# Kernel optimization log

Measured on AMD Instinct MI355X. Metric: run time of the kernel, lower is better.

Reference implementation:

```python
import jax, jax.numpy as jnp
import numpy as np

D_MODEL = 1024
N_HEAD = 16
L, B = 2048, 2


def setup_inputs() -> dict:
    key = jax.random.key(0)
    ks = jax.random.split(key, 11)
    inp = {
        "q": jax.random.normal(ks[0], (L, B, D_MODEL), dtype=jnp.float32),
        "k": jax.random.normal(ks[1], (L, B, D_MODEL), dtype=jnp.float32),
        "v": jax.random.normal(ks[2], (L, B, D_MODEL), dtype=jnp.float32),
        "sph": jax.random.uniform(ks[3], (B, N_HEAD, L, L), dtype=jnp.float32),
        "mask": jax.random.randint(ks[4], (B, L, L), 0, 2, dtype=jnp.int32),
        # learned params (torch Linear stores W of shape [out, in]; y = x @ W.T)
        "Wq": jax.random.normal(ks[5], (D_MODEL, D_MODEL), dtype=jnp.float32) * (1.0 / np.sqrt(D_MODEL)),
        "Wk": jax.random.normal(ks[6], (D_MODEL, D_MODEL), dtype=jnp.float32) * (1.0 / np.sqrt(D_MODEL)),
        "Wv": jax.random.normal(ks[7], (D_MODEL, D_MODEL), dtype=jnp.float32) * (1.0 / np.sqrt(D_MODEL)),
        "Wfc": jax.random.normal(ks[8], (D_MODEL, D_MODEL), dtype=jnp.float32) * (1.0 / np.sqrt(D_MODEL)),
        "gamma": jnp.ones((D_MODEL,), dtype=jnp.float32),
        "beta": jnp.zeros((D_MODEL,), dtype=jnp.float32),
    }
    return inp


def reference(q, k, v, sph, mask, Wq, Wk, Wv, Wfc, gamma, beta):
    # q, k, v: [L, B, D]  ->  batch-first [B, L, D]
    n_head = N_HEAD
    Lq, Bb, D = q.shape
    d_k = D // n_head
    x_q = jnp.transpose(q, (1, 0, 2))
    x_k = jnp.transpose(k, (1, 0, 2))
    x_v = jnp.transpose(v, (1, 0, 2))
    residual = x_q  # [B, L, D]

    # projections (no bias), split heads: [B, H, L, d_k]
    qh = (x_q @ Wq.T).reshape(Bb, Lq, n_head, d_k).transpose(0, 2, 1, 3)
    kh = (x_k @ Wk.T).reshape(Bb, Lq, n_head, d_k).transpose(0, 2, 1, 3)
    vh = (x_v @ Wv.T).reshape(Bb, Lq, n_head, d_k).transpose(0, 2, 1, 3)

    scale = jnp.asarray(d_k, qh.dtype) ** 0.5
    attn = jnp.einsum('bhqd,bhkd->bhqk', qh / scale, kh)
    attn = attn * sph                                   # spatial decay modulation
    attn = jnp.where(mask[:, None, :, :] == 0, jnp.asarray(-1e9, attn.dtype), attn)
    p_attn = jax.nn.softmax(attn, axis=-1)              # dropout is identity in eval

    out = jnp.einsum('bhqk,bhkd->bhqd', p_attn, vh)     # [B, H, L, d_k]
    out = out.transpose(0, 2, 1, 3).reshape(Bb, Lq, D)
    out = out @ Wfc.T + residual                        # fc (no bias) + residual

    # LayerNorm(eps=1e-6)
    mu = jnp.mean(out, axis=-1, keepdims=True)
    var = jnp.var(out, axis=-1, keepdims=True)
    out = (out - mu) * jax.lax.rsqrt(var + 1e-6) * gamma + beta

    return jnp.transpose(out, (1, 0, 2)), p_attn
```

## Files before the change

kernel.cpp:

```cpp
#include <hip/hip_runtime.h>
#include <hip/hip_bf16.h>

#define LL 2048
#define BB 2
#define DD 1024
#define HH 16
#define DKk 64

typedef __attribute__((ext_vector_type(8))) short s8v;
typedef __attribute__((ext_vector_type(8))) unsigned short u8v;
typedef __attribute__((ext_vector_type(4))) float f4v;

__device__ __forceinline__ ushort f2b(float f){
  union { __hip_bfloat16 h; ushort u; } c; c.h = __float2bfloat16(f); return c.u;
}
__device__ __forceinline__ float b2f(ushort u){
  union { __hip_bfloat16 h; ushort u; } c; c.u = u; return __bfloat162float(c.h);
}
__device__ __forceinline__ void nts4(float* p, f4v v){ __builtin_nontemporal_store(v, (f4v*)p); }

__global__ __launch_bounds__(256) void pack_all_kernel(
    const float* __restrict__ q, const float* __restrict__ k, const float* __restrict__ v,
    const float* __restrict__ Wq, const float* __restrict__ Wk,
    const float* __restrict__ Wv, const float* __restrict__ Wfc,
    const int* __restrict__ mask,
    ushort* __restrict__ xq, ushort* __restrict__ xk, ushort* __restrict__ xv,
    ushort* __restrict__ wb, unsigned* __restrict__ mbitsT){
  int blk = blockIdx.x;
  if (blk < 2048){
    int t = blk*256 + threadIdx.x;
    int m = t >> 7;
    int dc = (t & 127) << 3;
    int b = m >> 11, l = m & (LL-1);
    size_t src = ((size_t)(l*BB + b) << 10) + dc;
    size_t dst = ((size_t)m << 10) + dc;
    #pragma unroll
    for (int i=0;i<3;++i){
      const float* ss = (i==0)?q:(i==1)?k:v;
      ushort* dd = (i==0)?xq:(i==1)?xk:xv;
      float4 a = *(const float4*)(ss+src);
      float4 bb = *(const float4*)(ss+src+4);
      u8v o;
      o[0]=f2b(a.x); o[1]=f2b(a.y); o[2]=f2b(a.z); o[3]=f2b(a.w);
      o[4]=f2b(bb.x);o[5]=f2b(bb.y);o[6]=f2b(bb.z);o[7]=f2b(bb.w);
      *(u8v*)(dd+dst) = o;
    }
  } else if (blk < 4096){
    int t = (blk-2048)*256 + threadIdx.x;
    int which = t >> 17;
    size_t idx = (size_t)(t & 131071) << 3;
    const float* s = (which==0)?Wq:(which==1)?Wk:(which==2)?Wv:Wfc;
    float4 a = *(const float4*)(s+idx);
    float4 b4 = *(const float4*)(s+idx+4);
    u8v o;
    o[0]=f2b(a.x);o[1]=f2b(a.y);o[2]=f2b(a.z);o[3]=f2b(a.w);
    o[4]=f2b(b4.x);o[5]=f2b(b4.y);o[6]=f2b(b4.z);o[7]=f2b(b4.w);
    *(u8v*)(wb + ((size_t)which<<20) + idx) = o;
  } else {
    int t = (blk-4096)*256 + threadIdx.x;
    int rowg = t >> 6, lane = t & 63;
    const int* mrow = mask + ((size_t)rowg<<11);
    unsigned mw = 0;
    #pragma unroll
    for (int c=0;c<4;++c){
      const int* p = mrow + (c<<9) + (lane<<3);
      int4 a = *(const int4*)p; int4 b4 = *(const int4*)(p+4);
      unsigned by = (a.x&1)|((a.y&1)<<1)|((a.z&1)<<2)|((a.w&1)<<3)
                  |((b4.x&1)<<4)|((b4.y&1)<<5)|((b4.z&1)<<6)|((b4.w&1)<<7);
      mw |= by << (c*8);
    }
    mbitsT[((size_t)rowg<<6) + lane] = mw;
  }
}

__device__ __forceinline__ void gemm_body(
    const ushort* __restrict__ A, const ushort* __restrict__ W,
    ushort* __restrict__ outb, float* __restrict__ outf, const float* __restrict__ resid,
    int mode, float scale){
  __shared__ ushort As[4096];
  __shared__ ushort Bs[4096];
  int tid = threadIdx.x;
  int w = tid>>6, lane = tid&63, lane15 = lane&15, g = lane>>4;
  int m0 = blockIdx.y<<7, n0 = blockIdx.x<<7;
  int wr = w>>1, wc = w&1;
  f4v z4 = {0.f,0.f,0.f,0.f};
  f4v acc[4][4];
  #pragma unroll
  for (int i=0;i<4;++i)
    #pragma unroll
    for (int j=0;j<4;++j) acc[i][j] = z4;

  int f0 = tid, f1 = 256 + tid;
  int r0 = f0>>2, c0 = (f0&3)<<3;
  int r1 = f1>>2, c1 = (f1&3)<<3;
  for (int k0=0; k0<1024; k0+=32){
    *(s8v*)&As[(r0<<5)+c0] = *(const s8v*)&A[((size_t)(m0+r0)<<10) + k0 + c0];
    *(s8v*)&As[(r1<<5)+c1] = *(const s8v*)&A[((size_t)(m0+r1)<<10) + k0 + c1];
    *(s8v*)&Bs[(r0<<5)+c0] = *(const s8v*)&W[((size_t)(n0+r0)<<10) + k0 + c0];
    *(s8v*)&Bs[(r1<<5)+c1] = *(const s8v*)&W[((size_t)(n0+r1)<<10) + k0 + c1];
    __syncthreads();
    s8v af[4], bf_[4];
    #pragma unroll
    for (int mi=0;mi<4;++mi) af[mi] = *(s8v*)&As[((wr*64 + mi*16 + lane15)<<5) + (g<<3)];
    #pragma unroll
    for (int ni=0;ni<4;++ni) bf_[ni] = *(s8v*)&Bs[((wc*64 + ni*16 + lane15)<<5) + (g<<3)];
    #pragma unroll
    for (int mi=0;mi<4;++mi)
      #pragma unroll
      for (int ni=0;ni<4;++ni)
        acc[mi][ni] = __builtin_amdgcn_mfma_f32_16x16x32_bf16(af[mi], bf_[ni], acc[mi][ni], 0,0,0);
    __syncthreads();
  }
  #pragma unroll
  for (int mi=0;mi<4;++mi){
    #pragma unroll
    for (int ni=0;ni<4;++ni){
      int mbase = m0 + wr*64 + mi*16 + (g<<2);
      int ncol  = n0 + wc*64 + ni*16 + lane15;
      if (mode==0){
        int b=mbase>>11, h=ncol>>6, j=ncol&63;
        size_t o = (((size_t)(b*HH+h)*LL + (mbase&2047))<<6) + j;
        #pragma unroll
        for (int r=0;r<4;++r) outb[o + ((size_t)r<<6)] = f2b(acc[mi][ni][r]*scale);
      } else if (mode==2){
        int b=mbase>>11, h=ncol>>6, j=ncol&63;
        ushort4 pk = make_ushort4(f2b(acc[mi][ni][0]), f2b(acc[mi][ni][1]),
                                  f2b(acc[mi][ni][2]), f2b(acc[mi][ni][3]));
        *(ushort4*)&outb[(((size_t)(b*HH+h)*DKk + j)<<11) + (mbase&2047)] = pk;
      } else {
        int b=mbase>>11, l2=mbase&2047;
        #pragma unroll
        for (int r=0;r<4;++r)
          outf[((size_t)(mbase+r)<<10)+ncol] =
              acc[mi][ni][r] + resid[((size_t)((l2+r)*BB + b)<<10) + ncol];
      }
    }
  }
}

__global__ __launch_bounds__(256) void gemm_qkv_kernel(
    const ushort* __restrict__ xq, const ushort* __restrict__ xk, const ushort* __restrict__ xv,
    const ushort* __restrict__ wb, ushort* __restrict__ Qh, ushort* __restrict__ Kh, ushort* __restrict__ Vt){
  int z = blockIdx.z;
  const ushort* A = (z==0)?xq:(z==1)?xk:xv;
  const ushort* W = wb + ((size_t)z<<20);
  ushort* outb = (z==0)?Qh:(z==1)?Kh:Vt;
  int mode = (z==2)?2:0;
  float scale = (z==0)?0.125f:1.0f;
  gemm_body(A, W, outb, nullptr, nullptr, mode, scale);
}

__global__ __launch_bounds__(256) void gemm_fc_kernel(
    const ushort* __restrict__ ao, const ushort* __restrict__ wfc,
    const float* __restrict__ resid, float* __restrict__ fco){
  gemm_body(ao, wfc, nullptr, fco, resid, 3, 1.0f);
}

__global__ __launch_bounds__(1024, 4) void attn_kernel(
    const ushort* __restrict__ Qh, const ushort* __restrict__ Kh, const ushort* __restrict__ Vt,
    const float* __restrict__ sph, const unsigned* __restrict__ mbitsT,
    float* __restrict__ p_out, ushort* __restrict__ attn_out){
  extern __shared__ char smem[];
  float* pbuf   = (float*)(smem + 65536);
  float* redsum = (float*)(smem + 65536 + 13056);
  int tid = threadIdx.x, w = tid>>6, lane = tid&63, lane15 = lane&15, g = lane>>4;
  int bid = blockIdx.x;
  int pair = bid & 31;
  int qt = bid >> 5;
  int h = pair & 15, b = pair >> 4;
  int q0 = qt<<4;
  size_t bh = (size_t)b*HH + h;
  int row = w;
  int qrow = q0 + row;

  const float* sph_r = sph + ((bh*LL + qrow)<<11);
  int colbase = lane<<3;
  f4v sA0,sA1,sB0,sB1,sC0,sC1,sD0,sD1;
  {
    const float* p0 = sph_r + colbase;
    const float* p1 = p0 + 1024;
    asm volatile("global_load_dwordx4 %0, %1, off"             : "=v"(sA0) : "v"(p0));
    asm volatile("global_load_dwordx4 %0, %1, off offset:16"   : "=v"(sA1) : "v"(p0));
    asm volatile("global_load_dwordx4 %0, %1, off offset:2048" : "=v"(sB0) : "v"(p0));
    asm volatile("global_load_dwordx4 %0, %1, off offset:2064" : "=v"(sB1) : "v"(p0));
    asm volatile("global_load_dwordx4 %0, %1, off"             : "=v"(sC0) : "v"(p1));
    asm volatile("global_load_dwordx4 %0, %1, off offset:16"   : "=v"(sC1) : "v"(p1));
    asm volatile("global_load_dwordx4 %0, %1, off offset:2048" : "=v"(sD0) : "v"(p1));
    asm volatile("global_load_dwordx4 %0, %1, off offset:2064" : "=v"(sD1) : "v"(p1));
  }
  unsigned mw = mbitsT[(((size_t)b*LL + qrow)<<6) + lane];

  const ushort* Qbase = Qh + ((bh*LL + q0 + lane15)<<6) + (g<<3);
  s8v qa0 = *(const s8v*)Qbase;
  s8v qa1 = *(const s8v*)(Qbase + 32);
  const ushort* Kp = Kh + ((bh*LL + (w<<7) + lane15)<<6) + (g<<3);
  #pragma unroll
  for (int cc=0; cc<8; ++cc){
    const ushort* Kb = Kp + (cc<<10);
    s8v kb0 = *(const s8v*)Kb;
    s8v kb1 = *(const s8v*)(Kb + 32);
    f4v cacc = {0.f,0.f,0.f,0.f};
    cacc = __builtin_amdgcn_mfma_f32_16x16x32_bf16(qa0, kb0, cacc, 0,0,0);
    cacc = __builtin_amdgcn_mfma_f32_16x16x32_bf16(qa1, kb1, cacc, 0,0,0);
    int colb = (((w<<3)+cc)<<5) + (lane15<<1);
    #pragma unroll
    for (int r=0;r<4;++r){
      int rr2 = (g<<2)+r;
      *(ushort*)(smem + (rr2<<12) + (colb ^ ((rr2&7)<<4))) = f2b(cacc[r]);
    }
  }
  __syncthreads();

  asm volatile("s_waitcnt vmcnt(0)"
    : "+v"(sA0),"+v"(sA1),"+v"(sB0),"+v"(sB1),
      "+v"(sC0),"+v"(sC1),"+v"(sD0),"+v"(sD1));
  __builtin_amdgcn_sched_barrier(0);
  f4v spl[4][2] = {{sA0,sA1},{sB0,sB1},{sC0,sC1},{sD0,sD1}};

  int rswz = (row&7)<<4;
  char* Srow = smem + (row<<12);
  float sum = 0.f;
  u8v ev[4];
  #pragma unroll
  for (int c2=0;c2<4;++c2){
    int boff = (((colbase + (c2<<9))<<1) ^ rswz);
    s8v sv = *(s8v*)(Srow + boff);
    f4v p0 = spl[c2][0], p1 = spl[c2][1];
    unsigned m8 = (mw >> (c2*8));
    float e[8];
    e[0] = (m8&1)   ? __expf(b2f((ushort)sv[0])*p0[0]) : 0.f;
    e[1] = (m8&2)   ? __expf(b2f((ushort)sv[1])*p0[1]) : 0.f;
    e[2] = (m8&4)   ? __expf(b2f((ushort)sv[2])*p0[2]) : 0.f;
    e[3] = (m8&8)   ? __expf(b2f((ushort)sv[3])*p0[3]) : 0.f;
    e[4] = (m8&16)  ? __expf(b2f((ushort)sv[4])*p1[0]) : 0.f;
    e[5] = (m8&32)  ? __expf(b2f((ushort)sv[5])*p1[1]) : 0.f;
    e[6] = (m8&64)  ? __expf(b2f((ushort)sv[6])*p1[2]) : 0.f;
    e[7] = (m8&128) ? __expf(b2f((ushort)sv[7])*p1[3]) : 0.f;
    u8v ov;
    #pragma unroll
    for (int j=0;j<8;++j){ sum += e[j]; ov[j] = f2b(e[j]); }
    ev[c2] = ov;
    *(u8v*)(Srow + boff) = ov;
  }
  #pragma unroll
  for (int off=1; off<64; off<<=1) sum += __shfl_xor(sum, off, 64);
  if (lane==0) redsum[row] = sum;

  float inv = 1.0f / sum;
  float* prow_p = p_out + ((bh*LL + qrow)<<11);
  #pragma unroll
  for (int c2=0;c2<4;++c2){
    int col = colbase + (c2<<9);
    f4v o0, o1;
    o0[0]=b2f((ushort)ev[c2][0])*inv; o0[1]=b2f((ushort)ev[c2][1])*inv;
    o0[2]=b2f((ushort)ev[c2][2])*inv; o0[3]=b2f((ushort)ev[c2][3])*inv;
    o1[0]=b2f((ushort)ev[c2][4])*inv; o1[1]=b2f((ushort)ev[c2][5])*inv;
    o1[2]=b2f((ushort)ev[c2][6])*inv; o1[3]=b2f((ushort)ev[c2][7])*inv;
    nts4(prow_p + col, o0);
    nts4(prow_p + col + 4, o1);
  }

  int ds = w & 3, kq = w >> 2;
  const ushort* Vb = Vt + ((bh*DKk + (ds<<4) + lane15)<<11) + (kq<<9) + (g<<3);
  s8v vb[4];
  #pragma unroll
  for (int i=0;i<4;++i) vb[i] = *(const s8v*)(Vb + (i<<5));
  __syncthreads();

  f4v oacc = {0.f,0.f,0.f,0.f};
  char* Sa = smem + (lane15<<12);
  int aswz = (lane15&7)<<4;
  s8v pan = *(s8v*)(Sa + (((kq<<10) + (g<<4)) ^ aswz));
  #pragma unroll
  for (int it=0; it<16; ++it){
    s8v pa = pan;
    if (it<15) pan = *(s8v*)(Sa + (((kq<<10) + ((it+1)<<6) + (g<<4)) ^ aswz));
    s8v vcur = vb[it&3];
    if (it<12) vb[it&3] = *(const s8v*)(Vb + ((it+4)<<5));
    oacc = __builtin_amdgcn_mfma_f32_16x16x32_bf16(pa, vcur, oacc, 0,0,0);
  }
  if (kq){
    float* pp = pbuf + ((kq-1)*1088);
    #pragma unroll
    for (int r=0;r<4;++r) pp[((g<<2)+r)*68 + (ds<<4) + lane15] = oacc[r];
  }
  __syncthreads();
  if (kq==0){
    #pragma unroll
    for (int p3=0;p3<3;++p3){
      float* pp = pbuf + p3*1088;
      #pragma unroll
      for (int r=0;r<4;++r) oacc[r] += pp[((g<<2)+r)*68 + (ds<<4) + lane15];
    }
    #pragma unroll
    for (int r=0;r<4;++r){
      int qr = (g<<2)+r;
      float val = oacc[r] / redsum[qr];
      attn_out[((size_t)(b*LL + q0 + qr)<<10) + (h<<6) + (ds<<4) + lane15] = f2b(val);
    }
  }
}

__global__ __launch_bounds__(256) void ln_kernel(const float* __restrict__ fc,
    const float* __restrict__ gamma, const float* __restrict__ beta, float* __restrict__ out){
  __shared__ float rs[4], rq[4];
  int m = blockIdx.x, tid = threadIdx.x;
  int d0 = tid<<2;
  float4 x = *(const float4*)(fc + ((size_t)m<<10) + d0);
  float s = x.x+x.y+x.z+x.w;
  float sq = x.x*x.x+x.y*x.y+x.z*x.z+x.w*x.w;
  #pragma unroll
  for (int off=32; off; off>>=1){ s += __shfl_xor(s,off,64); sq += __shfl_xor(sq,off,64); }
  if ((tid&63)==0){ rs[tid>>6]=s; rq[tid>>6]=sq; }
  __syncthreads();
  float ts = rs[0]+rs[1]+rs[2]+rs[3];
  float tq = rq[0]+rq[1]+rq[2]+rq[3];
  float mu = ts*(1.0f/1024.0f);
  float var = tq*(1.0f/1024.0f) - mu*mu;
  float rr = rsqrtf(var + 1e-6f);
  float4 gm = *(const float4*)(gamma + d0);
  float4 bt = *(const float4*)(beta + d0);
  float4 y;
  y.x=(x.x-mu)*rr*gm.x+bt.x;
  y.y=(x.y-mu)*rr*gm.y+bt.y;
  y.z=(x.z-mu)*rr*gm.z+bt.z;
  y.w=(x.w-mu)*rr*gm.w+bt.w;
  int b=m>>11, l2=m&2047;
  *(float4*)(out + ((size_t)(l2*BB+b)<<10) + d0) = y;
}

extern "C" void kernel_launch(void* const* d_in, const int* in_sizes, int n_in,
                              void* d_out, int out_size, void* d_ws, size_t ws_size,
                              hipStream_t stream){
  const float* q    = (const float*)d_in[0];
  const float* k    = (const float*)d_in[1];
  const float* v    = (const float*)d_in[2];
  const float* sph  = (const float*)d_in[3];
  const int*   mask = (const int*)d_in[4];
  const float* Wq   = (const float*)d_in[5];
  const float* Wk   = (const float*)d_in[6];
  const float* Wv   = (const float*)d_in[7];
  const float* Wfc  = (const float*)d_in[8];
  const float* gamma= (const float*)d_in[9];
  const float* beta = (const float*)d_in[10];
  float* outp  = (float*)d_out;
  float* p_out = outp + 4194304;

  char* ws = (char*)d_ws;
  ushort* xq  = (ushort*)(ws);
  ushort* xk  = (ushort*)(ws + 8388608);
  ushort* xv  = (ushort*)(ws + 16777216);
  ushort* wb  = (ushort*)(ws + 25165824);
  ushort* Qh  = (ushort*)(ws + 33554432);
  ushort* Kh  = (ushort*)(ws + 41943040);
  ushort* Vt  = (ushort*)(ws + 50331648);
  ushort* ao  = (ushort*)(ws + 58720256);
  float*  fco = (float*)(ws + 67108864);
  unsigned* mbitsT = (unsigned*)(ws + 83886080);

  pack_all_kernel<<<5120,256,0,stream>>>(q,k,v,Wq,Wk,Wv,Wfc,mask,xq,xk,xv,wb,mbitsT);
  gemm_qkv_kernel<<<dim3(8,32,3),256,0,stream>>>(xq,xk,xv,wb,Qh,Kh,Vt);
  attn_kernel<<<4096,1024,78784,stream>>>(Qh,Kh,Vt,sph,mbitsT,p_out,ao);
  gemm_fc_kernel<<<dim3(8,32),256,0,stream>>>(ao, wb + 3145728, q, fco);
  ln_kernel<<<4096,256,0,stream>>>(fco, gamma, beta, outp);
}
```

Baseline: 534.0 us.

## Split fused attention into separate QK, softmax and PV kernels via bf16 score buffer

Replaces the single fused attention kernel with three kernels: QK^T writes bf16 scores to a large workspace buffer, a row-wise softmax kernel applies sph and the mask, exponentiates, writes p_attn and stores unnormalized exps back, and a PV kernel multiplies by V and divides by row sums. The aim is to give each phase better occupancy and memory access patterns than the monolithic kernel. In exchange it adds roughly 256 MB of extra global memory traffic for the intermediate score matrix, plus two more kernel launches. The softmax also skips max subtraction, which risks overflow, and the path only runs when the workspace is large enough.

```diff
diff --git a/kernel.cpp b/kernel.cpp
--- a/kernel.cpp
+++ b/kernel.cpp
@@ -18,6 +18,7 @@
   union { __hip_bfloat16 h; ushort u; } c; c.u = u; return __bfloat162float(c.h);
 }
 __device__ __forceinline__ void nts4(float* p, f4v v){ __builtin_nontemporal_store(v, (f4v*)p); }
+__device__ __forceinline__ f4v ntl4(const float* p){ return __builtin_nontemporal_load((const f4v*)p); }
 
 __global__ __launch_bounds__(256) void pack_all_kernel(
     const float* __restrict__ q, const float* __restrict__ k, const float* __restrict__ v,
@@ -156,6 +157,178 @@
   gemm_body(ao, wfc, nullptr, fco, resid, 3, 1.0f);
 }
 
+__global__ __launch_bounds__(1024, 4) void qk_kernel(
+    const ushort* __restrict__ Qh, const ushort* __restrict__ Kh, ushort* __restrict__ Se){
+  __shared__ char smem[65536];
+  int tid = threadIdx.x, w = tid>>6, lane = tid&63, lane15 = lane&15, g = lane>>4;
+  int bid = blockIdx.x;
+  int pair = bid & 31;
+  int qt = bid >> 5;
+  int h = pair & 15, b = pair >> 4;
+  int q0 = qt<<4;
+  size_t bh = (size_t)b*HH + h;
+
+  const ushort* Qbase = Qh + ((bh*LL + q0 + lane15)<<6) + (g<<3);
+  s8v qa0 = *(const s8v*)Qbase;
+  s8v qa1 = *(const s8v*)(Qbase + 32);
+  const ushort* Kp = Kh + ((bh*LL + (w<<7) + lane15)<<6) + (g<<3);
+  #pragma unroll
+  for (int cc=0; cc<8; ++cc){
+    const ushort* Kb = Kp + (cc<<10);
+    s8v kb0 = *(const s8v*)Kb;
+    s8v kb1 = *(const s8v*)(Kb + 32);
+    f4v cacc = {0.f,0.f,0.f,0.f};
+    cacc = __builtin_amdgcn_mfma_f32_16x16x32_bf16(qa0, kb0, cacc, 0,0,0);
+    cacc = __builtin_amdgcn_mfma_f32_16x16x32_bf16(qa1, kb1, cacc, 0,0,0);
+    int colb = (((w<<3)+cc)<<5) + (lane15<<1);
+    #pragma unroll
+    for (int r=0;r<4;++r){
+      int rr2 = (g<<2)+r;
+      *(ushort*)(smem + (rr2<<12) + (colb ^ ((rr2&7)<<4))) = f2b(cacc[r]);
+    }
+  }
+  __syncthreads();
+  int rswz = (w&7)<<4;
+  char* Srow = smem + (w<<12);
+  ushort* So = Se + ((bh*LL + q0 + w)<<11);
+  #pragma unroll
+  for (int c=0;c<4;++c){
+    s8v v = *(s8v*)(Srow + (((c<<10) + (lane<<4)) ^ rswz));
+    *(s8v*)(So + (c<<9) + (lane<<3)) = v;
+  }
+}
+
+__global__ __launch_bounds__(256, 4) void sm_kernel(
+    ushort* __restrict__ Se, const float* __restrict__ sph,
+    const unsigned* __restrict__ mbitsT,
+    float* __restrict__ rowsums, float* __restrict__ p_out){
+  int tid = threadIdx.x, lane = tid&63, w = tid>>6;
+  int r = blockIdx.x*4 + w;
+  int b = r >> 15, qq = r & 2047;
+  ushort* Srow = Se + ((size_t)r<<11);
+  const float* srow = sph + ((size_t)r<<11);
+  unsigned mw = mbitsT[(((size_t)(b<<11) + qq)<<6) + lane];
+
+  s8v sv0 = *(const s8v*)(Srow + (lane<<3));
+  s8v sv1 = *(const s8v*)(Srow + 512 + (lane<<3));
+  s8v sv2 = *(const s8v*)(Srow + 1024 + (lane<<3));
+  s8v sv3 = *(const s8v*)(Srow + 1536 + (lane<<3));
+  f4v sp0 = ntl4(srow + (lane<<3));
+  f4v sp1 = ntl4(srow + (lane<<3) + 4);
+  f4v sp2 = ntl4(srow + 512 + (lane<<3));
+  f4v sp3 = ntl4(srow + 512 + (lane<<3) + 4);
+  f4v sp4 = ntl4(srow + 1024 + (lane<<3));
+  f4v sp5 = ntl4(srow + 1024 + (lane<<3) + 4);
+  f4v sp6 = ntl4(srow + 1536 + (lane<<3));
+  f4v sp7 = ntl4(srow + 1536 + (lane<<3) + 4);
+
+  float sum = 0.f;
+  u8v ev[4];
+  s8v svs[4] = {sv0, sv1, sv2, sv3};
+  f4v sps[8] = {sp0, sp1, sp2, sp3, sp4, sp5, sp6, sp7};
+  #pragma unroll
+  for (int c=0;c<4;++c){
+    s8v sv = svs[c];
+    f4v p0 = sps[2*c], p1 = sps[2*c+1];
+    unsigned m8 = mw >> (c*8);
+    float e[8];
+    e[0] = (m8&1)   ? __expf(b2f((ushort)sv[0])*p0[0]) : 0.f;
+    e[1] = (m8&2)   ? __expf(b2f((ushort)sv[1])*p0[1]) : 0.f;
+    e[2] = (m8&4)   ? __expf(b2f((ushort)sv[2])*p0[2]) : 0.f;
+    e[3] = (m8&8)   ? __expf(b2f((ushort)sv[3])*p0[3]) : 0.f;
+    e[4] = (m8&16)  ? __expf(b2f((ushort)sv[4])*p1[0]) : 0.f;
+    e[5] = (m8&32)  ? __expf(b2f((ushort)sv[5])*p1[1]) : 0.f;
+    e[6] = (m8&64)  ? __expf(b2f((ushort)sv[6])*p1[2]) : 0.f;
+    e[7] = (m8&128) ? __expf(b2f((ushort)sv[7])*p1[3]) : 0.f;
+    u8v ov;
+    #pragma unroll
+    for (int j=0;j<8;++j){ sum += e[j]; ov[j] = f2b(e[j]); }
+    ev[c] = ov;
+  }
+  #pragma unroll
+  for (int off=1; off<64; off<<=1) sum += __shfl_xor(sum, off, 64);
+  if (lane==0) rowsums[r] = sum;
+  float inv = 1.0f / sum;
+
+  float* prow = p_out + ((size_t)r<<11);
+  #pragma unroll
+  for (int c=0;c<4;++c){
+    *(u8v*)(Srow + (c<<9) + (lane<<3)) = ev[c];
+    f4v o0, o1;
+    o0[0]=b2f(ev[c][0])*inv; o0[1]=b2f(ev[c][1])*inv;
+    o0[2]=b2f(ev[c][2])*inv; o0[3]=b2f(ev[c][3])*inv;
+    o1[0]=b2f(ev[c][4])*inv; o1[1]=b2f(ev[c][5])*inv;
+    o1[2]=b2f(ev[c][6])*inv; o1[3]=b2f(ev[c][7])*inv;
+    nts4(prow + (c<<9) + (lane<<3), o0);
+    nts4(prow + (c<<9) + (lane<<3) + 4, o1);
+  }
+}
+
+__global__ __launch_bounds__(1024, 4) void pv_kernel(
+    const ushort* __restrict__ Se, const ushort* __restrict__ Vt,
+    const float* __restrict__ rowsums, ushort* __restrict__ attn_out){
+  __shared__ char smem[65536];
+  __shared__ float pbuf[3*1088];
+  __shared__ float redsum[16];
+  int tid = threadIdx.x, w = tid>>6, lane = tid&63, lane15 = lane&15, g = lane>>4;
+  int bid = blockIdx.x;
+  int pair = bid & 31;
+  int qt = bid >> 5;
+  int h = pair & 15, b = pair >> 4;
+  int q0 = qt<<4;
+  size_t bh = (size_t)b*HH + h;
+
+  int rswz = (w&7)<<4;
+  const ushort* er = Se + ((bh*LL + q0 + w)<<11);
+  char* Srow = smem + (w<<12);
+  #pragma unroll
+  for (int c=0;c<4;++c){
+    s8v v = *(const s8v*)(er + (c<<9) + (lane<<3));
+    *(s8v*)(Srow + (((c<<10) + (lane<<4)) ^ rswz)) = v;
+  }
+  if (tid < 16) redsum[tid] = rowsums[bh*LL + q0 + tid];
+
+  int ds = w & 3, kq = w >> 2;
+  const ushort* Vb = Vt + ((bh*DKk + (ds<<4) + lane15)<<11) + (kq<<9) + (g<<3);
+  s8v vb[4];
+  #pragma unroll
+  for (int i=0;i<4;++i) vb[i] = *(const s8v*)(Vb + (i<<5));
+  __syncthreads();
+
+  f4v oacc = {0.f,0.f,0.f,0.f};
+  char* Sa = smem + (lane15<<12);
+  int aswz = (lane15&7)<<4;
+  s8v pan = *(s8v*)(Sa + (((kq<<10) + (g<<4)) ^ aswz));
+  #pragma unroll
+  for (int it=0; it<16; ++it){
+    s8v pa = pan;
+    if (it<15) pan = *(s8v*)(Sa + (((kq<<10) + ((it+1)<<6) + (g<<4)) ^ aswz));
+    s8v vcur = vb[it&3];
+    if (it<12) vb[it&3] = *(const s8v*)(Vb + ((it+4)<<5));
+    oacc = __builtin_amdgcn_mfma_f32_16x16x32_bf16(pa, vcur, oacc, 0,0,0);
+  }
+  if (kq){
+    float* pp = pbuf + (kq-1)*1088;
+    #pragma unroll
+    for (int r=0;r<4;++r) pp[((g<<2)+r)*68 + (ds<<4) + lane15] = oacc[r];
+  }
+  __syncthreads();
+  if (kq==0){
+    #pragma unroll
+    for (int p3=0;p3<3;++p3){
+      float* pp = pbuf + p3*1088;
+      #pragma unroll
+      for (int r=0;r<4;++r) oacc[r] += pp[((g<<2)+r)*68 + (ds<<4) + lane15];
+    }
+    #pragma unroll
+    for (int r=0;r<4;++r){
+      int qr = (g<<2)+r;
+      float val = oacc[r] / redsum[qr];
+      attn_out[((size_t)(b*LL + q0 + qr)<<10) + (h<<6) + (ds<<4) + lane15] = f2b(val);
+    }
+  }
+}
+
 __global__ __launch_bounds__(1024, 4) void attn_kernel(
     const ushort* __restrict__ Qh, const ushort* __restrict__ Kh, const ushort* __restrict__ Vt,
     const float* __restrict__ sph, const unsigned* __restrict__ mbitsT,
@@ -357,10 +530,20 @@
   ushort* ao  = (ushort*)(ws + 58720256);
   float*  fco = (float*)(ws + 67108864);
   unsigned* mbitsT = (unsigned*)(ws + 83886080);
+  float* rowsums = (float*)(ws + 84934656);
+  ushort* Se = (ushort*)(ws + 85196800);
+
+  const size_t WS_NEEDED = 85196800ull + 268435456ull;
 
   pack_all_kernel<<<5120,256,0,stream>>>(q,k,v,Wq,Wk,Wv,Wfc,mask,xq,xk,xv,wb,mbitsT);
   gemm_qkv_kernel<<<dim3(8,32,3),256,0,stream>>>(xq,xk,xv,wb,Qh,Kh,Vt);
-  attn_kernel<<<4096,1024,78784,stream>>>(Qh,Kh,Vt,sph,mbitsT,p_out,ao);
+  if (ws_size >= WS_NEEDED){
+    qk_kernel<<<4096,1024,0,stream>>>(Qh,Kh,Se);
+    sm_kernel<<<16384,256,0,stream>>>(Se,sph,mbitsT,rowsums,p_out);
+    pv_kernel<<<4096,1024,0,stream>>>(Se,Vt,rowsums,ao);
+  } else {
+    attn_kernel<<<4096,1024,78784,stream>>>(Qh,Kh,Vt,sph,mbitsT,p_out,ao);
+  }
   gemm_fc_kernel<<<dim3(8,32),256,0,stream>>>(ao, wb + 3145728, q, fco);
   ln_kernel<<<4096,256,0,stream>>>(fco, gamma, beta, outp);
 }
```

Result: slower. 662.6 us (+24.1%).
